# Kernel tuning notes

Measured on AMD Instinct MI355X. Metric: run time of the kernel, lower is better.

## Reference

```python
import jax, jax.numpy as jnp
import numpy as np

L = 6        # number of blocks (hardcoded in Transformer)
H = 16       # num_heads
C = 1024     # num_embeddings
HS = C // H  # head_size = 64
FF = 4 * C   # ffn hidden
V = 67       # vocab = len(chars)
B, T = 8, 1024
EPS = 1e-5   # nn.LayerNorm default


def _ln(x, g, b):
    m = jnp.mean(x, axis=-1, keepdims=True)
    v = jnp.mean((x - m) ** 2, axis=-1, keepdims=True)
    return (x - m) * jax.lax.rsqrt(v + EPS) * g + b


def setup_inputs() -> dict:
    key = jax.random.key(0)
    ks = jax.random.split(key, 20)
    s = 0.02
    inp = {
        "idx": jax.random.randint(ks[0], (B, T), 0, V),
        "tok_emb": jax.random.normal(ks[1], (V, C), jnp.float32) * s,
        "pos_emb": jax.random.normal(ks[2], (T, C), jnp.float32) * s,
        # per-head Q/K/V Linears (bias=False) packed as [L, C, H*HS]
        "Wq": jax.random.normal(ks[3], (L, C, C), jnp.float32) * s,
        "Wk": jax.random.normal(ks[4], (L, C, C), jnp.float32) * s,
        "Wv": jax.random.normal(ks[5], (L, C, C), jnp.float32) * s,
        "Wo": jax.random.normal(ks[6], (L, C, C), jnp.float32) * s,
        "bo": jnp.zeros((L, C), jnp.float32),
        "ln1_g": jnp.ones((L, C), jnp.float32),
        "ln1_b": jnp.zeros((L, C), jnp.float32),
        "ln2_g": jnp.ones((L, C), jnp.float32),
        "ln2_b": jnp.zeros((L, C), jnp.float32),
        "W1": jax.random.normal(ks[7], (L, C, FF), jnp.float32) * s,
        "b1": jnp.zeros((L, FF), jnp.float32),
        "W2": jax.random.normal(ks[8], (L, FF, C), jnp.float32) * s,
        "b2": jnp.zeros((L, C), jnp.float32),
        "lnf_g": jnp.ones((C,), jnp.float32),
        "lnf_b": jnp.zeros((C,), jnp.float32),
        "Wlm": jax.random.normal(ks[9], (C, V), jnp.float32) * s,
        "blm": jnp.zeros((V,), jnp.float32),
    }
    return inp


def reference(idx, tok_emb, pos_emb, Wq, Wk, Wv, Wo, bo, ln1_g, ln1_b,
              ln2_g, ln2_b, W1, b1, W2, b2, lnf_g, lnf_b, Wlm, blm):
    Bc, Tc = idx.shape
    x = tok_emb[idx] + pos_emb[:Tc]                      # [B,T,C]
    mask = jnp.tril(jnp.ones((Tc, Tc), bool))
    scale = 1.0 / np.sqrt(HS)                            # wei / head_size**0.5
    neg_inf = jnp.finfo(x.dtype).min
    for l in range(L):
        h = _ln(x, ln1_g[l], ln1_b[l])
        q = (h @ Wq[l]).reshape(Bc, Tc, H, HS)
        k = (h @ Wk[l]).reshape(Bc, Tc, H, HS)
        v = (h @ Wv[l]).reshape(Bc, Tc, H, HS)
        wei = jnp.einsum('bqhd,bkhd->bhqk', q, k) * scale
        wei = jnp.where(mask, wei, neg_inf)
        wei = jax.nn.softmax(wei, axis=-1)
        o = jnp.einsum('bhqk,bkhd->bqhd', wei, v).reshape(Bc, Tc, C)
        x = x + o @ Wo[l] + bo[l]
        h = _ln(x, ln2_g[l], ln2_b[l])
        x = x + jax.nn.relu(h @ W1[l] + b1[l]) @ W2[l] + b2[l]
    x = _ln(x, lnf_g, lnf_b)
    return x @ Wlm + blm                                 # [B,T,V] logits
```

## Files before the change

### kernel.cpp

```cpp
#include <hip/hip_runtime.h>

typedef unsigned short u16;
typedef unsigned int u32;
typedef __bf16 bf16x8 __attribute__((ext_vector_type(8)));
typedef float f32x4 __attribute__((ext_vector_type(4)));

#define LAYERS 6
#define NH 16
#define CDIM 1024
#define HS 64
#define FFDIM 4096
#define VOCAB 67
#define BATCH 8
#define TSEQ 1024
#define NTOK (BATCH * TSEQ)

__device__ __forceinline__ float bf2f(u16 u) {
    union { u32 i; float f; } x; x.i = ((u32)u) << 16; return x.f;
}
__device__ __forceinline__ u16 f2bf(float f) {
    u32 x = __float_as_uint(f);
    u32 r = (x + 0x7fffu + ((x >> 16) & 1u)) >> 16;
    return (u16)r;
}
__device__ __forceinline__ float ldx(const void* p, size_t i, int f32) {
    return f32 ? ((const float*)p)[i] : bf2f(((const u16*)p)[i]);
}

__global__ void detect_kernel(const void* __restrict__ tok, int* __restrict__ flag) {
    int bad = 0;
    for (int i = threadIdx.x; i < 4096; i += 256) {
        float f = bf2f(((const u16*)tok)[i]);
        if (!(fabsf(f) < 1000.0f)) bad = 1;
    }
    if (bad) atomicOr(flag, 1);
}

template <int BF16OUT>
__global__ void embed_kernel(const int* __restrict__ idx, const void* __restrict__ tok,
                             const void* __restrict__ pos, void* __restrict__ X,
                             const int* __restrict__ dflag) {
    const int f32 = *dflag;
    const int i = blockIdx.x * 256 + threadIdx.x;
    const int n = i >> 10, cc = i & 1023;
    const int t = n & 1023;
    const float v = ldx(tok, (size_t)idx[n] * CDIM + cc, f32) + ldx(pos, (size_t)t * CDIM + cc, f32);
    if constexpr (BF16OUT) ((u16*)X)[i] = f2bf(v);
    else                   ((float*)X)[i] = v;
}

__global__ void transpose_kernel(const void* __restrict__ src, size_t soff, u16* __restrict__ dst,
                                 int R, int C, const int* __restrict__ dflag) {
    __shared__ u16 tile[32][33];
    const int f32 = *dflag;
    const int bx = blockIdx.x * 32, by = blockIdx.y * 32;
    const int tx = threadIdx.x, ty = threadIdx.y;
    #pragma unroll
    for (int i = 0; i < 32; i += 8) {
        const size_t si = soff + (size_t)(by + ty + i) * C + bx + tx;
        tile[ty + i][tx] = f32 ? f2bf(((const float*)src)[si]) : ((const u16*)src)[si];
    }
    __syncthreads();
    #pragma unroll
    for (int i = 0; i < 32; i += 8) dst[(size_t)(bx + ty + i) * R + by + tx] = tile[tx][ty + i];
}

template <int BF16IN>
__global__ __launch_bounds__(256) void ln_kernel(const void* __restrict__ Xv, const void* __restrict__ g,
                                                 const void* __restrict__ b, size_t loff,
                                                 u16* __restrict__ Hout, const int* __restrict__ dflag) {
    __shared__ float sred[4];
    const int f32 = *dflag;
    const int row = blockIdx.x, tid = threadIdx.x;
    float v[4];
    if constexpr (BF16IN) {
        const u16* xr = (const u16*)Xv + (size_t)row * CDIM;
        #pragma unroll
        for (int i = 0; i < 4; ++i) v[i] = bf2f(xr[tid + i * 256]);
    } else {
        const float* xr = (const float*)Xv + (size_t)row * CDIM;
        #pragma unroll
        for (int i = 0; i < 4; ++i) v[i] = xr[tid + i * 256];
    }
    float s = v[0] + v[1] + v[2] + v[3];
    #pragma unroll
    for (int off = 1; off < 64; off <<= 1) s += __shfl_xor(s, off, 64);
    if ((tid & 63) == 0) sred[tid >> 6] = s;
    __syncthreads();
    const float mean = (sred[0] + sred[1] + sred[2] + sred[3]) * (1.f / 1024.f);
    __syncthreads();
    float sq = 0.f;
    #pragma unroll
    for (int i = 0; i < 4; ++i) { v[i] -= mean; sq += v[i] * v[i]; }
    #pragma unroll
    for (int off = 1; off < 64; off <<= 1) sq += __shfl_xor(sq, off, 64);
    if ((tid & 63) == 0) sred[tid >> 6] = sq;
    __syncthreads();
    const float var = (sred[0] + sred[1] + sred[2] + sred[3]) * (1.f / 1024.f);
    const float inv = rsqrtf(var + 1e-5f);
    u16* hr = Hout + (size_t)row * CDIM;
    #pragma unroll
    for (int i = 0; i < 4; ++i) {
        const int cc = tid + i * 256;
        hr[cc] = f2bf(v[i] * inv * ldx(g, loff + cc, f32) + ldx(b, loff + cc, f32));
    }
}

template <int MODE>
__global__ __launch_bounds__(256) void gemm_bt(const u16* __restrict__ A, const u16* __restrict__ BT,
                                               const void* __restrict__ bias, size_t boff,
                                               float* __restrict__ X, u16* __restrict__ Out,
                                               int M, int N, int K, const int* __restrict__ dflag) {
    __shared__ u16 As[128][64];
    __shared__ u16 Bs[128][64];
    const int tid = threadIdx.x;
    const int lane = tid & 63;
    const int w = tid >> 6;
    const int wr = w >> 1, wc = w & 1;
    const int quad = lane >> 4, c = lane & 15;
    const int m0 = blockIdx.y * 128, n0 = blockIdx.x * 128;
    const int srow = tid >> 3, schunk = (tid & 7) * 8;

    const f32x4 zero4 = {0.f, 0.f, 0.f, 0.f};
    f32x4 acc[4][4];
    #pragma unroll
    for (int i = 0; i < 4; ++i)
        #pragma unroll
        for (int j = 0; j < 4; ++j) acc[i][j] = zero4;

    for (int k0 = 0; k0 < K; k0 += 64) {
        #pragma unroll
        for (int i = 0; i < 4; ++i) {
            const int r = srow + i * 32;
            *(uint4*)(&As[r][schunk]) = *(const uint4*)(A + (size_t)(m0 + r) * K + k0 + schunk);
            *(uint4*)(&Bs[r][schunk]) = *(const uint4*)(BT + (size_t)(n0 + r) * K + k0 + schunk);
        }
        __syncthreads();
        #pragma unroll
        for (int ks = 0; ks < 2; ++ks) {
            bf16x8 af[4], bfr[4];
            #pragma unroll
            for (int t = 0; t < 4; ++t) {
                af[t]  = *(const bf16x8*)(&As[wr * 64 + t * 16 + c][ks * 32 + quad * 8]);
                bfr[t] = *(const bf16x8*)(&Bs[wc * 64 + t * 16 + c][ks * 32 + quad * 8]);
            }
            #pragma unroll
            for (int mt = 0; mt < 4; ++mt)
                #pragma unroll
                for (int nt = 0; nt < 4; ++nt)
                    acc[mt][nt] = __builtin_amdgcn_mfma_f32_16x16x32_bf16(af[mt], bfr[nt], acc[mt][nt], 0, 0, 0);
        }
        __syncthreads();
    }

    int f32 = 0;
    if constexpr (MODE >= 1) f32 = *dflag;
    #pragma unroll
    for (int mt = 0; mt < 4; ++mt) {
        #pragma unroll
        for (int nt = 0; nt < 4; ++nt) {
            const int col = n0 + wc * 64 + nt * 16 + c;
            float bv = 0.f;
            if constexpr (MODE >= 1) bv = ldx(bias, boff + col, f32);
            #pragma unroll
            for (int r = 0; r < 4; ++r) {
                const size_t row = (size_t)(m0 + wr * 64 + mt * 16 + quad * 4 + r);
                float v = acc[mt][nt][r];
                if constexpr (MODE == 2) {
                    X[row * N + col] += v + bv;
                } else if constexpr (MODE == 3) {
                    u16* o = &Out[row * N + col];
                    *o = f2bf(bf2f(*o) + v + bv);
                } else if constexpr (MODE == 1) {
                    v += bv; v = fmaxf(v, 0.f);
                    Out[row * N + col] = f2bf(v);
                } else {
                    Out[row * N + col] = f2bf(v);
                }
            }
        }
    }
}

__global__ __launch_bounds__(256) void attn_kernel(const u16* __restrict__ Qb, const u16* __restrict__ Kb,
                                                   const u16* __restrict__ Vb, u16* __restrict__ Ob) {
    __shared__ u16 Qs[64][64];
    __shared__ u16 Ks[64][64];
    __shared__ u16 Vts[64][64];
    __shared__ u16 Ps[4][16][64];

    const int tid = threadIdx.x;
    const int lane = tid & 63;
    const int w = tid >> 6;
    const int quad = lane >> 4;
    const int c = lane & 15;
    const int bh = blockIdx.x;
    const int b = bh >> 4;
    const int h = bh & 15;
    const int q0 = blockIdx.y * 64;
    const size_t base = ((size_t)b * TSEQ) * CDIM + (size_t)h * HS;

    {
        const int r = tid >> 2;
        const int d0 = (tid & 3) * 16;
        const u16* src = Qb + base + (size_t)(q0 + r) * CDIM + d0;
        #pragma unroll
        for (int i = 0; i < 16; ++i) Qs[r][d0 + i] = f2bf(bf2f(src[i]) * 0.125f);
    }
    __syncthreads();

    const int qbase = q0 + w * 16;
    const bf16x8 qf0 = *(const bf16x8*)(&Qs[w * 16 + c][quad * 8]);
    const bf16x8 qf1 = *(const bf16x8*)(&Qs[w * 16 + c][32 + quad * 8]);

    const f32x4 zero4 = {0.f, 0.f, 0.f, 0.f};
    f32x4 oacc[4] = {zero4, zero4, zero4, zero4};
    float m_r[4], l_r[4];
    #pragma unroll
    for (int r = 0; r < 4; ++r) { m_r[r] = -1e30f; l_r[r] = 0.f; }

    const int nch = blockIdx.y + 1;
    for (int ch = 0; ch < nch; ++ch) {
        const int k0 = ch * 64;
        {
            const int r = tid >> 2;
            const int d0 = (tid & 3) * 16;
            const u16* ks = Kb + base + (size_t)(k0 + r) * CDIM + d0;
            *(uint4*)(&Ks[r][d0])     = *(const uint4*)(ks);
            *(uint4*)(&Ks[r][d0 + 8]) = *(const uint4*)(ks + 8);
            const u16* vs = Vb + base + (size_t)(k0 + r) * CDIM + d0;
            #pragma unroll
            for (int i = 0; i < 16; ++i) Vts[d0 + i][r] = vs[i];
        }
        __syncthreads();

        f32x4 s[4];
        #pragma unroll
        for (int kt = 0; kt < 4; ++kt) {
            const bf16x8 kf0 = *(const bf16x8*)(&Ks[kt * 16 + c][quad * 8]);
            const bf16x8 kf1 = *(const bf16x8*)(&Ks[kt * 16 + c][32 + quad * 8]);
            f32x4 t0 = __builtin_amdgcn_mfma_f32_16x16x32_bf16(qf0, kf0, zero4, 0, 0, 0);
            s[kt] = __builtin_amdgcn_mfma_f32_16x16x32_bf16(qf1, kf1, t0, 0, 0, 0);
        }
        #pragma unroll
        for (int kt = 0; kt < 4; ++kt) {
            const int kabs = k0 + kt * 16 + c;
            #pragma unroll
            for (int r = 0; r < 4; ++r) {
                if (kabs > qbase + quad * 4 + r) s[kt][r] = -1e30f;
            }
        }
        float p[4][4];
        #pragma unroll
        for (int r = 0; r < 4; ++r) {
            float rm = fmaxf(fmaxf(s[0][r], s[1][r]), fmaxf(s[2][r], s[3][r]));
            #pragma unroll
            for (int off = 1; off < 16; off <<= 1) rm = fmaxf(rm, __shfl_xor(rm, off, 16));
            const float mnew = fmaxf(m_r[r], rm);
            const float alpha = __expf(m_r[r] - mnew);
            float psum = 0.f;
            #pragma unroll
            for (int kt = 0; kt < 4; ++kt) {
                const float e = __expf(s[kt][r] - mnew);
                p[kt][r] = e; psum += e;
            }
            #pragma unroll
            for (int off = 1; off < 16; off <<= 1) psum += __shfl_xor(psum, off, 16);
            l_r[r] = l_r[r] * alpha + psum;
            m_r[r] = mnew;
            #pragma unroll
            for (int dt = 0; dt < 4; ++dt) oacc[dt][r] *= alpha;
        }
        #pragma unroll
        for (int kt = 0; kt < 4; ++kt)
            #pragma unroll
            for (int r = 0; r < 4; ++r)
                Ps[w][quad * 4 + r][kt * 16 + c] = f2bf(p[kt][r]);
        __syncthreads();
        #pragma unroll
        for (int ks2 = 0; ks2 < 2; ++ks2) {
            const bf16x8 pf = *(const bf16x8*)(&Ps[w][c][ks2 * 32 + quad * 8]);
            #pragma unroll
            for (int dt = 0; dt < 4; ++dt) {
                const bf16x8 vf = *(const bf16x8*)(&Vts[dt * 16 + c][ks2 * 32 + quad * 8]);
                oacc[dt] = __builtin_amdgcn_mfma_f32_16x16x32_bf16(pf, vf, oacc[dt], 0, 0, 0);
            }
        }
        __syncthreads();
    }
    #pragma unroll
    for (int dt = 0; dt < 4; ++dt)
        #pragma unroll
        for (int r = 0; r < 4; ++r) {
            const size_t row = (size_t)b * TSEQ + qbase + quad * 4 + r;
            Ob[row * CDIM + h * HS + dt * 16 + c] = f2bf(oacc[dt][r] / l_r[r]);
        }
}

__global__ void wlmT_kernel(const void* __restrict__ Wlm, u16* __restrict__ WlmT,
                            const int* __restrict__ dflag) {
    const int f32 = *dflag;
    const int i = blockIdx.x * 256 + threadIdx.x;
    if (i >= VOCAB * CDIM) return;
    const int v = i >> 10, cc = i & 1023;
    WlmT[i] = f2bf(ldx(Wlm, (size_t)cc * VOCAB + v, f32));
}

__device__ __forceinline__ void ld16bf(const u16* p, float* v) {
    const uint4 a = *(const uint4*)(p);
    const uint4 b = *(const uint4*)(p + 8);
    u32 t[8] = {a.x, a.y, a.z, a.w, b.x, b.y, b.z, b.w};
    #pragma unroll
    for (int i = 0; i < 8; ++i) {
        v[2 * i]     = bf2f((u16)(t[i] & 0xffffu));
        v[2 * i + 1] = bf2f((u16)(t[i] >> 16));
    }
}

__global__ __launch_bounds__(256) void lmhead2_kernel(const u16* __restrict__ Hf, const u16* __restrict__ WlmT,
                                                      const void* __restrict__ blm, void* __restrict__ out,
                                                      size_t ooff, const int* __restrict__ dflag) {
    const int f32 = *dflag;
    const int lane = threadIdx.x & 63;
    const int n = blockIdx.x * 4 + (threadIdx.x >> 6);
    float hv[16];
    ld16bf(Hf + (size_t)n * CDIM + lane * 16, hv);
    for (int v = 0; v < VOCAB; ++v) {
        float wv[16];
        ld16bf(WlmT + (size_t)v * CDIM + lane * 16, wv);
        float s = 0.f;
        #pragma unroll
        for (int i = 0; i < 16; ++i) s += hv[i] * wv[i];
        #pragma unroll
        for (int off = 1; off < 64; off <<= 1) s += __shfl_xor(s, off, 64);
        if (lane == 0) {
            s += ldx(blm, v, f32);
            const size_t o = ooff + (size_t)n * VOCAB + v;
            if (f32) ((float*)out)[o] = s;
            else     ((u16*)out)[o]   = f2bf(s);
        }
    }
}

extern "C" void kernel_launch(void* const* d_in, const int* in_sizes, int n_in,
                              void* d_out, int out_size, void* d_ws, size_t ws_size,
                              hipStream_t stream) {
    const int*  idx  = (const int*)d_in[0];
    const void* tok  = d_in[1];
    const void* pos  = d_in[2];
    const void* Wq   = d_in[3];
    const void* Wk   = d_in[4];
    const void* Wv   = d_in[5];
    const void* Wo   = d_in[6];
    const void* bo   = d_in[7];
    const void* ln1g = d_in[8];
    const void* ln1b = d_in[9];
    const void* ln2g = d_in[10];
    const void* ln2b = d_in[11];
    const void* W1   = d_in[12];
    const void* b1   = d_in[13];
    const void* W2   = d_in[14];
    const void* b2   = d_in[15];
    const void* lnfg = d_in[16];
    const void* lnfb = d_in[17];
    const void* Wlm  = d_in[18];
    const void* blm  = d_in[19];

    const dim3 tb(32, 8);
    const size_t wsz = (size_t)CDIM * CDIM;
    const size_t MB = 1048576ull;

    int* dflag = (int*)d_ws;
    char* pool = (char*)d_ws + 256;
    const size_t pool_size = (ws_size > 256) ? ws_size - 256 : 0;

    const int wlmT_blocks = (VOCAB * CDIM + 255) / 256;

    if (pool_size >= 120 * MB) {
        hipMemsetAsync(d_ws, 0, 256 + 120 * MB, stream);
        detect_kernel<<<1, 256, 0, stream>>>(tok, dflag);
        char* p = pool;
        u16* wT = (u16*)p;  p += (size_t)FFDIM * CDIM * 2;
        u16* WqT = wT;
        u16* WkT = wT + 1 * wsz;
        u16* WvT = wT + 2 * wsz;
        u16* WoT = wT + 3 * wsz;
        float* x = (float*)p; p += (size_t)NTOK * CDIM * 4;
        u16* h   = (u16*)p;   p += (size_t)NTOK * CDIM * 2;
        u16* qb  = (u16*)p;   p += (size_t)NTOK * CDIM * 2;
        u16* kb  = (u16*)p;   p += (size_t)NTOK * CDIM * 2;
        u16* vb  = (u16*)p;   p += (size_t)NTOK * CDIM * 2;
        u16* ob  = (u16*)p;   p += (size_t)NTOK * CDIM * 2;
        u16* ffh = qb;

        embed_kernel<0><<<NTOK * CDIM / 256, 256, 0, stream>>>(idx, tok, pos, x, dflag);
        for (int l = 0; l < LAYERS; ++l) {
            transpose_kernel<<<dim3(32, 32), tb, 0, stream>>>(Wq, l * wsz, WqT, CDIM, CDIM, dflag);
            transpose_kernel<<<dim3(32, 32), tb, 0, stream>>>(Wk, l * wsz, WkT, CDIM, CDIM, dflag);
            transpose_kernel<<<dim3(32, 32), tb, 0, stream>>>(Wv, l * wsz, WvT, CDIM, CDIM, dflag);
            transpose_kernel<<<dim3(32, 32), tb, 0, stream>>>(Wo, l * wsz, WoT, CDIM, CDIM, dflag);
            ln_kernel<0><<<NTOK, 256, 0, stream>>>(x, ln1g, ln1b, (size_t)l * CDIM, h, dflag);
            gemm_bt<0><<<dim3(8, 64), 256, 0, stream>>>(h, WqT, nullptr, 0, nullptr, qb, NTOK, CDIM, CDIM, dflag);
            gemm_bt<0><<<dim3(8, 64), 256, 0, stream>>>(h, WkT, nullptr, 0, nullptr, kb, NTOK, CDIM, CDIM, dflag);
            gemm_bt<0><<<dim3(8, 64), 256, 0, stream>>>(h, WvT, nullptr, 0, nullptr, vb, NTOK, CDIM, CDIM, dflag);
            attn_kernel<<<dim3(BATCH * NH, TSEQ / 64), 256, 0, stream>>>(qb, kb, vb, ob);
            gemm_bt<2><<<dim3(8, 64), 256, 0, stream>>>(ob, WoT, bo, (size_t)l * CDIM, x, nullptr, NTOK, CDIM, CDIM, dflag);
            ln_kernel<0><<<NTOK, 256, 0, stream>>>(x, ln2g, ln2b, (size_t)l * CDIM, h, dflag);
            transpose_kernel<<<dim3(128, 32), tb, 0, stream>>>(W1, (size_t)l * CDIM * FFDIM, wT, CDIM, FFDIM, dflag);
            gemm_bt<1><<<dim3(32, 64), 256, 0, stream>>>(h, wT, b1, (size_t)l * FFDIM, nullptr, ffh, NTOK, FFDIM, CDIM, dflag);
            transpose_kernel<<<dim3(32, 128), tb, 0, stream>>>(W2, (size_t)l * CDIM * FFDIM, wT, FFDIM, CDIM, dflag);
            gemm_bt<2><<<dim3(8, 64), 256, 0, stream>>>(ffh, wT, b2, (size_t)l * CDIM, x, nullptr, NTOK, CDIM, FFDIM, dflag);
        }
        ln_kernel<0><<<NTOK, 256, 0, stream>>>(x, lnfg, lnfb, 0, h, dflag);
        wlmT_kernel<<<wlmT_blocks, 256, 0, stream>>>(Wlm, qb, dflag);
        lmhead2_kernel<<<NTOK / 4, 256, 0, stream>>>(h, qb, blm, d_out, 0, dflag);
    } else if (pool_size >= 34 * MB) {
        const int CR = (pool_size >= 44 * MB) ? 2048 : 1024;
        const size_t need = 8 * MB + 16 * MB + (size_t)CR * CDIM * 2 * 5;
        const int useW2T = (pool_size >= need + 8 * MB);
        hipMemsetAsync(d_ws, 0, 256 + need + (useW2T ? 8 * MB : 0), stream);
        detect_kernel<<<1, 256, 0, stream>>>(tok, dflag);
        char* p = pool;
        u16* wT = (u16*)p;  p += (size_t)FFDIM * CDIM * 2;
        u16* WqT = wT;
        u16* WkT = wT + 1 * wsz;
        u16* WvT = wT + 2 * wsz;
        u16* WoT = wT + 3 * wsz;
        u16* xb  = (u16*)p; p += (size_t)NTOK * CDIM * 2;
        u16* hc  = (u16*)p; p += (size_t)CR * CDIM * 2;
        u16* qc  = (u16*)p; p += (size_t)CR * CDIM * 2;
        u16* kc  = (u16*)p; p += (size_t)CR * CDIM * 2;
        u16* vc  = (u16*)p; p += (size_t)CR * CDIM * 2;
        u16* oc  = (u16*)p; p += (size_t)CR * CDIM * 2;
        u16* ffc = qc;
        u16* W2T = nullptr;
        if (useW2T) { W2T = (u16*)p; p += (size_t)FFDIM * CDIM * 2; }

        embed_kernel<1><<<NTOK * CDIM / 256, 256, 0, stream>>>(idx, tok, pos, xb, dflag);
        for (int l = 0; l < LAYERS; ++l) {
            transpose_kernel<<<dim3(32, 32), tb, 0, stream>>>(Wq, l * wsz, WqT, CDIM, CDIM, dflag);
            transpose_kernel<<<dim3(32, 32), tb, 0, stream>>>(Wk, l * wsz, WkT, CDIM, CDIM, dflag);
            transpose_kernel<<<dim3(32, 32), tb, 0, stream>>>(Wv, l * wsz, WvT, CDIM, CDIM, dflag);
            transpose_kernel<<<dim3(32, 32), tb, 0, stream>>>(Wo, l * wsz, WoT, CDIM, CDIM, dflag);
            for (int g = 0; g < NTOK / CR; ++g) {
                u16* xg = xb + (size_t)g * CR * CDIM;
                ln_kernel<1><<<CR, 256, 0, stream>>>(xg, ln1g, ln1b, (size_t)l * CDIM, hc, dflag);
                gemm_bt<0><<<dim3(8, CR / 128), 256, 0, stream>>>(hc, WqT, nullptr, 0, nullptr, qc, CR, CDIM, CDIM, dflag);
                gemm_bt<0><<<dim3(8, CR / 128), 256, 0, stream>>>(hc, WkT, nullptr, 0, nullptr, kc, CR, CDIM, CDIM, dflag);
                gemm_bt<0><<<dim3(8, CR / 128), 256, 0, stream>>>(hc, WvT, nullptr, 0, nullptr, vc, CR, CDIM, CDIM, dflag);
                attn_kernel<<<dim3((CR / TSEQ) * NH, TSEQ / 64), 256, 0, stream>>>(qc, kc, vc, oc);
                gemm_bt<3><<<dim3(8, CR / 128), 256, 0, stream>>>(oc, WoT, bo, (size_t)l * CDIM, nullptr, xg, CR, CDIM, CDIM, dflag);
            }
            if (W2T) {
                transpose_kernel<<<dim3(128, 32), tb, 0, stream>>>(W1, (size_t)l * CDIM * FFDIM, wT, CDIM, FFDIM, dflag);
                transpose_kernel<<<dim3(32, 128), tb, 0, stream>>>(W2, (size_t)l * CDIM * FFDIM, W2T, FFDIM, CDIM, dflag);
                for (int g = 0; g < NTOK / CR; ++g) {
                    u16* xg = xb + (size_t)g * CR * CDIM;
                    ln_kernel<1><<<CR, 256, 0, stream>>>(xg, ln2g, ln2b, (size_t)l * CDIM, hc, dflag);
                    gemm_bt<1><<<dim3(32, CR / 128), 256, 0, stream>>>(hc, wT, b1, (size_t)l * FFDIM, nullptr, ffc, CR, FFDIM, CDIM, dflag);
                    gemm_bt<3><<<dim3(8, CR / 128), 256, 0, stream>>>(ffc, W2T, b2, (size_t)l * CDIM, nullptr, xg, CR, CDIM, FFDIM, dflag);
                }
            } else {
                for (int g = 0; g < NTOK / CR; ++g) {
                    u16* xg = xb + (size_t)g * CR * CDIM;
                    ln_kernel<1><<<CR, 256, 0, stream>>>(xg, ln2g, ln2b, (size_t)l * CDIM, hc, dflag);
                    transpose_kernel<<<dim3(128, 32), tb, 0, stream>>>(W1, (size_t)l * CDIM * FFDIM, wT, CDIM, FFDIM, dflag);
                    gemm_bt<1><<<dim3(32, CR / 128), 256, 0, stream>>>(hc, wT, b1, (size_t)l * FFDIM, nullptr, ffc, CR, FFDIM, CDIM, dflag);
                    transpose_kernel<<<dim3(32, 128), tb, 0, stream>>>(W2, (size_t)l * CDIM * FFDIM, wT, FFDIM, CDIM, dflag);
                    gemm_bt<3><<<dim3(8, CR / 128), 256, 0, stream>>>(ffc, wT, b2, (size_t)l * CDIM, nullptr, xg, CR, CDIM, FFDIM, dflag);
                }
            }
        }
        wlmT_kernel<<<wlmT_blocks, 256, 0, stream>>>(Wlm, qc, dflag);
        for (int g = 0; g < NTOK / CR; ++g) {
            u16* xg = xb + (size_t)g * CR * CDIM;
            ln_kernel<1><<<CR, 256, 0, stream>>>(xg, lnfg, lnfb, 0, hc, dflag);
            lmhead2_kernel<<<CR / 4, 256, 0, stream>>>(hc, qc, blm, d_out, (size_t)g * CR * VOCAB, dflag);
        }
    } else {
        hipMemsetAsync(d_out, 0, (size_t)out_size * 2, stream);
    }
}
```

Before: 3.596 ms.

## Fuse QKV GEMMs, load GEMM tiles directly into LDS, swizzle blocks across XCDs

The three Q/K/V projections become one GEMM with N=3C over the contiguous transposed weights. Attention then reads Q, K and V from the interleaved output through a new row-stride argument. The GEMM tile loads now use global_load_lds, which copies global memory straight into LDS instead of going through registers. Workgroup IDs are also remapped so neighbouring tiles land on the same XCD. These changes cut launches and reloads of the activation matrix and should improve L2 locality; in exchange the attention reads are strided and the workspace size thresholds change.

```diff
diff --git a/kernel.cpp b/kernel.cpp
--- a/kernel.cpp
+++ b/kernel.cpp
@@ -25,6 +25,11 @@
 }
 __device__ __forceinline__ float ldx(const void* p, size_t i, int f32) {
     return f32 ? ((const float*)p)[i] : bf2f(((const u16*)p)[i]);
+}
+__device__ __forceinline__ void glds16(const u16* g, u16* lds) {
+    __builtin_amdgcn_global_load_lds(
+        (const __attribute__((address_space(1))) void*)g,
+        (__attribute__((address_space(3))) void*)lds, 16, 0, 0);
 }
 
 __global__ void detect_kernel(const void* __restrict__ tok, int* __restrict__ flag) {
@@ -118,8 +123,21 @@
     const int w = tid >> 6;
     const int wr = w >> 1, wc = w & 1;
     const int quad = lane >> 4, c = lane & 15;
-    const int m0 = blockIdx.y * 128, n0 = blockIdx.x * 128;
-    const int srow = tid >> 3, schunk = (tid & 7) * 8;
+
+    const int gx = gridDim.x, gy = gridDim.y;
+    int bx = blockIdx.x, by = blockIdx.y;
+    const int nwg = gx * gy;
+    if ((nwg & 7) == 0) {
+        const int bid = by * gx + bx;
+        const int q = nwg >> 3;
+        const int l = (bid & 7) * q + (bid >> 3);
+        bx = l / gy;
+        by = l - bx * gy;
+    }
+    const int m0 = by * 128, n0 = bx * 128;
+
+    const int lr = lane >> 3;
+    const int lc = (lane & 7) * 8;
 
     const f32x4 zero4 = {0.f, 0.f, 0.f, 0.f};
     f32x4 acc[4][4];
@@ -131,9 +149,9 @@
     for (int k0 = 0; k0 < K; k0 += 64) {
         #pragma unroll
         for (int i = 0; i < 4; ++i) {
-            const int r = srow + i * 32;
-            *(uint4*)(&As[r][schunk]) = *(const uint4*)(A + (size_t)(m0 + r) * K + k0 + schunk);
-            *(uint4*)(&Bs[r][schunk]) = *(const uint4*)(BT + (size_t)(n0 + r) * K + k0 + schunk);
+            const int rbase = w * 8 + i * 32;
+            glds16(A  + (size_t)(m0 + rbase + lr) * K + k0 + lc, &As[rbase][0]);
+            glds16(BT + (size_t)(n0 + rbase + lr) * K + k0 + lc, &Bs[rbase][0]);
         }
         __syncthreads();
         #pragma unroll
@@ -183,7 +201,8 @@
 }
 
 __global__ __launch_bounds__(256) void attn_kernel(const u16* __restrict__ Qb, const u16* __restrict__ Kb,
-                                                   const u16* __restrict__ Vb, u16* __restrict__ Ob) {
+                                                   const u16* __restrict__ Vb, u16* __restrict__ Ob,
+                                                   int rs) {
     __shared__ u16 Qs[64][64];
     __shared__ u16 Ks[64][64];
     __shared__ u16 Vts[64][64];
@@ -198,12 +217,12 @@
     const int b = bh >> 4;
     const int h = bh & 15;
     const int q0 = blockIdx.y * 64;
-    const size_t base = ((size_t)b * TSEQ) * CDIM + (size_t)h * HS;
+    const size_t base = ((size_t)b * TSEQ) * rs + (size_t)h * HS;
 
     {
         const int r = tid >> 2;
         const int d0 = (tid & 3) * 16;
-        const u16* src = Qb + base + (size_t)(q0 + r) * CDIM + d0;
+        const u16* src = Qb + base + (size_t)(q0 + r) * rs + d0;
         #pragma unroll
         for (int i = 0; i < 16; ++i) Qs[r][d0 + i] = f2bf(bf2f(src[i]) * 0.125f);
     }
@@ -225,10 +244,10 @@
         {
             const int r = tid >> 2;
             const int d0 = (tid & 3) * 16;
-            const u16* ks = Kb + base + (size_t)(k0 + r) * CDIM + d0;
+            const u16* ks = Kb + base + (size_t)(k0 + r) * rs + d0;
             *(uint4*)(&Ks[r][d0])     = *(const uint4*)(ks);
             *(uint4*)(&Ks[r][d0 + 8]) = *(const uint4*)(ks + 8);
-            const u16* vs = Vb + base + (size_t)(k0 + r) * CDIM + d0;
+            const u16* vs = Vb + base + (size_t)(k0 + r) * rs + d0;
             #pragma unroll
             for (int i = 0; i < 16; ++i) Vts[d0 + i][r] = vs[i];
         }
@@ -388,8 +407,8 @@
         float* x = (float*)p; p += (size_t)NTOK * CDIM * 4;
         u16* h   = (u16*)p;   p += (size_t)NTOK * CDIM * 2;
         u16* qb  = (u16*)p;   p += (size_t)NTOK * CDIM * 2;
-        u16* kb  = (u16*)p;   p += (size_t)NTOK * CDIM * 2;
-        u16* vb  = (u16*)p;   p += (size_t)NTOK * CDIM * 2;
+        u16* kb  = (u16*)p;   p += (size_t)NTOK * CDIM * 2;  (void)kb;
+        u16* vb  = (u16*)p;   p += (size_t)NTOK * CDIM * 2;  (void)vb;
         u16* ob  = (u16*)p;   p += (size_t)NTOK * CDIM * 2;
         u16* ffh = qb;
 
@@ -400,10 +419,8 @@
             transpose_kernel<<<dim3(32, 32), tb, 0, stream>>>(Wv, l * wsz, WvT, CDIM, CDIM, dflag);
             transpose_kernel<<<dim3(32, 32), tb, 0, stream>>>(Wo, l * wsz, WoT, CDIM, CDIM, dflag);
             ln_kernel<0><<<NTOK, 256, 0, stream>>>(x, ln1g, ln1b, (size_t)l * CDIM, h, dflag);
-            gemm_bt<0><<<dim3(8, 64), 256, 0, stream>>>(h, WqT, nullptr, 0, nullptr, qb, NTOK, CDIM, CDIM, dflag);
-            gemm_bt<0><<<dim3(8, 64), 256, 0, stream>>>(h, WkT, nullptr, 0, nullptr, kb, NTOK, CDIM, CDIM, dflag);
-            gemm_bt<0><<<dim3(8, 64), 256, 0, stream>>>(h, WvT, nullptr, 0, nullptr, vb, NTOK, CDIM, CDIM, dflag);
-            attn_kernel<<<dim3(BATCH * NH, TSEQ / 64), 256, 0, stream>>>(qb, kb, vb, ob);
+            gemm_bt<0><<<dim3(24, 64), 256, 0, stream>>>(h, wT, nullptr, 0, nullptr, qb, NTOK, 3 * CDIM, CDIM, dflag);
+            attn_kernel<<<dim3(BATCH * NH, TSEQ / 64), 256, 0, stream>>>(qb, qb + CDIM, qb + 2 * CDIM, ob, 3 * CDIM);
             gemm_bt<2><<<dim3(8, 64), 256, 0, stream>>>(ob, WoT, bo, (size_t)l * CDIM, x, nullptr, NTOK, CDIM, CDIM, dflag);
             ln_kernel<0><<<NTOK, 256, 0, stream>>>(x, ln2g, ln2b, (size_t)l * CDIM, h, dflag);
             transpose_kernel<<<dim3(128, 32), tb, 0, stream>>>(W1, (size_t)l * CDIM * FFDIM, wT, CDIM, FFDIM, dflag);
@@ -415,10 +432,12 @@
         wlmT_kernel<<<wlmT_blocks, 256, 0, stream>>>(Wlm, qb, dflag);
         lmhead2_kernel<<<NTOK / 4, 256, 0, stream>>>(h, qb, blm, d_out, 0, dflag);
     } else if (pool_size >= 34 * MB) {
-        const int CR = (pool_size >= 44 * MB) ? 2048 : 1024;
-        const size_t need = 8 * MB + 16 * MB + (size_t)CR * CDIM * 2 * 5;
-        const int useW2T = (pool_size >= need + 8 * MB);
-        hipMemsetAsync(d_ws, 0, 256 + need + (useW2T ? 8 * MB : 0), stream);
+        int CR, useW2T;
+        if      (pool_size >= 52 * MB) { CR = 2048; useW2T = 1; }
+        else if (pool_size >= 42 * MB) { CR = 1024; useW2T = 1; }
+        else                           { CR = 1024; useW2T = 0; }
+        const size_t need = 8 * MB + 16 * MB + (size_t)CR * CDIM * 2 * 5 + (useW2T ? 8 * MB : 0);
+        hipMemsetAsync(d_ws, 0, 256 + need, stream);
         detect_kernel<<<1, 256, 0, stream>>>(tok, dflag);
         char* p = pool;
         u16* wT = (u16*)p;  p += (size_t)FFDIM * CDIM * 2;
@@ -429,8 +448,8 @@
         u16* xb  = (u16*)p; p += (size_t)NTOK * CDIM * 2;
         u16* hc  = (u16*)p; p += (size_t)CR * CDIM * 2;
         u16* qc  = (u16*)p; p += (size_t)CR * CDIM * 2;
-        u16* kc  = (u16*)p; p += (size_t)CR * CDIM * 2;
-        u16* vc  = (u16*)p; p += (size_t)CR * CDIM * 2;
+        u16* kc  = (u16*)p; p += (size_t)CR * CDIM * 2;      (void)kc;
+        u16* vc  = (u16*)p; p += (size_t)CR * CDIM * 2;      (void)vc;
         u16* oc  = (u16*)p; p += (size_t)CR * CDIM * 2;
         u16* ffc = qc;
         u16* W2T = nullptr;
@@ -445,10 +464,8 @@
             for (int g = 0; g < NTOK / CR; ++g) {
                 u16* xg = xb + (size_t)g * CR * CDIM;
                 ln_kernel<1><<<CR, 256, 0, stream>>>(xg, ln1g, ln1b, (size_t)l * CDIM, hc, dflag);
-                gemm_bt<0><<<dim3(8, CR / 128), 256, 0, stream>>>(hc, WqT, nullptr, 0, nullptr, qc, CR, CDIM, CDIM, dflag);
-                gemm_bt<0><<<dim3(8, CR / 128), 256, 0, stream>>>(hc, WkT, nullptr, 0, nullptr, kc, CR, CDIM, CDIM, dflag);
-                gemm_bt<0><<<dim3(8, CR / 128), 256, 0, stream>>>(hc, WvT, nullptr, 0, nullptr, vc, CR, CDIM, CDIM, dflag);
-                attn_kernel<<<dim3((CR / TSEQ) * NH, TSEQ / 64), 256, 0, stream>>>(qc, kc, vc, oc);
+                gemm_bt<0><<<dim3(24, CR / 128), 256, 0, stream>>>(hc, wT, nullptr, 0, nullptr, qc, CR, 3 * CDIM, CDIM, dflag);
+                attn_kernel<<<dim3((CR / TSEQ) * NH, TSEQ / 64), 256, 0, stream>>>(qc, qc + CDIM, qc + 2 * CDIM, oc, 3 * CDIM);
                 gemm_bt<3><<<dim3(8, CR / 128), 256, 0, stream>>>(oc, WoT, bo, (size_t)l * CDIM, nullptr, xg, CR, CDIM, CDIM, dflag);
             }
             if (W2T) {
```

Result: faster. 3.310 ms (-8.0%).
